# Kernel optimization log

Hardware: AMD Instinct MI355X
Metric: run time of the kernel (lower is better)

## Reference

```python
import jax, jax.numpy as jnp
import numpy as np

DIM = 1024
N_HEADS = 16
HEAD_DIM = DIM // N_HEADS
LORA_DIM = 16
B, T = 4, 1024


def _rope(x):
    # x: [B, H, T, D] with D even; rotate first/second halves (torch impl style)
    D = x.shape[-1]
    half = D // 2
    theta = 1.0 / (10000.0 ** (jnp.arange(0, D, 2, dtype=jnp.float32) / D))  # [D/2]
    pos = jnp.arange(x.shape[-2], dtype=jnp.float32)                         # [T]
    pt = pos[:, None] * theta[None, :]                                       # [T, D/2]
    sin, cos = jnp.sin(pt), jnp.cos(pt)
    xr, xi = x[..., :half], x[..., half:]
    return jnp.concatenate([xr * cos - xi * sin, xr * sin + xi * cos], axis=-1)


def setup_inputs() -> dict:
    key = jax.random.key(0)
    ks = jax.random.split(key, 16)
    def n(k, shape, std=0.02):
        return jax.random.normal(k, shape, jnp.float32) * std
    return {
        "x": jax.random.normal(ks[0], (B, T, DIM), jnp.float32),
        "q_w": n(ks[1], (DIM, DIM)),
        "k_w": n(ks[2], (DIM, DIM)),
        "v_w": n(ks[3], (DIM, DIM)),
        "q_a": n(ks[4], (LORA_DIM, DIM), 0.001),
        "q_b": n(ks[5], (DIM, LORA_DIM), 0.001),
        "q_l": jax.random.normal(ks[6], (DIM,), jnp.float32),
        "k_a": n(ks[7], (LORA_DIM, DIM), 0.001),
        "k_b": n(ks[8], (DIM, LORA_DIM), 0.001),
        "k_l": jax.random.normal(ks[9], (DIM,), jnp.float32),
        "v_a": n(ks[10], (LORA_DIM, DIM), 0.001),
        "v_b": n(ks[11], (DIM, LORA_DIM), 0.001),
        "v_l": jax.random.normal(ks[12], (DIM,), jnp.float32),
        "proj_w": n(ks[13], (DIM, DIM)),
        "proj_b": n(ks[14], (DIM,)),
    }


def reference(x, q_w, k_w, v_w, q_a, q_b, q_l, k_a, k_b, k_l,
              v_a, v_b, v_l, proj_w, proj_b):
    Bb, Tt, C = x.shape
    # token shift: xx[t] = x[t-1], xx[0] = 0 (ZeroPad2d((0,0,1,-1)))
    xx = jnp.pad(x, ((0, 0), (1, 0), (0, 0)))[:, :Tt]
    xxx = xx - x

    def lora(a, b, lam):
        return lam + jnp.tanh(x @ a.T) @ b.T  # [B,T,C]

    q = (x + xxx * lora(q_a, q_b, q_l)) @ q_w.T
    k = (x + xxx * lora(k_a, k_b, k_l)) @ k_w.T
    v = (x + xxx * lora(v_a, v_b, v_l)) @ v_w.T

    def split_heads(t):
        return t.reshape(Bb, Tt, N_HEADS, HEAD_DIM).transpose(0, 2, 1, 3)  # [B,H,T,D]

    q = _rope(split_heads(q))
    k = _rope(split_heads(k))
    v = split_heads(v)

    scale = 1.0 / np.sqrt(HEAD_DIM).astype(np.float32)
    scores = jnp.einsum('bhqd,bhkd->bhqk', q, k) * scale
    causal = jnp.tril(jnp.ones((Tt, Tt), dtype=bool))
    scores = jnp.where(causal, scores, jnp.float32(-1e30))
    att = jax.nn.softmax(scores, axis=-1)
    out = jnp.einsum('bhqk,bhkd->bhqd', att, v)
    out = out.transpose(0, 2, 1, 3).reshape(Bb, Tt, C)
    return out @ proj_w.T + proj_b
```

## Files before the change

### kernel.cpp

```cpp
#include <hip/hip_runtime.h>
#include <hip/hip_bf16.h>

typedef __hip_bfloat16 bf16;
typedef __attribute__((ext_vector_type(8))) short bf16x8;
typedef __attribute__((ext_vector_type(4))) float f32x4;

typedef const __attribute__((address_space(1))) unsigned int* gp_t;
typedef __attribute__((address_space(3))) unsigned int* lp_t;

__device__ __forceinline__ bf16 tobf(float f) { return __float2bfloat16(f); }
__device__ __forceinline__ float tof(bf16 h) { return __bfloat162float(h); }

__device__ __forceinline__ short bfbits(float f) {
    bf16 h = __float2bfloat16(f);
    return *reinterpret_cast<short*>(&h);
}
__device__ __forceinline__ bf16x8 pack8(float4 a, float4 b) {
    bf16x8 r;
    r[0] = bfbits(a.x); r[1] = bfbits(a.y); r[2] = bfbits(a.z); r[3] = bfbits(a.w);
    r[4] = bfbits(b.x); r[5] = bfbits(b.y); r[6] = bfbits(b.z); r[7] = bfbits(b.w);
    return r;
}

__device__ __forceinline__ void gload_lds16(const void* g, void* l) {
    __builtin_amdgcn_global_load_lds((gp_t)g, (lp_t)l, 16, 0, 0);
}

__global__ __launch_bounds__(256) void lora_t_wconv(
    const float* x,
    const float* qa, const float* ka, const float* va,
    const float* qw, const float* kw, const float* vw, const float* pw,
    bf16* wdst, float* Tg) {
    int tid = threadIdx.x;

    if (blockIdx.x >= 256) {
        int cblk = blockIdx.x - 256;
        int m = cblk >> 7;
        const float* src = m == 0 ? qw : (m == 1 ? kw : (m == 2 ? vw : pw));
        bf16* dst = wdst + (size_t)m * (1u << 20);
        int off = (cblk & 127) * 8192;
#pragma unroll
        for (int u = 0; u < 8; ++u) {
            int i = off + u * 1024 + tid * 4;
            float4 f = *(const float4*)(src + i);
            ushort4 o4;
            o4.x = (unsigned short)bfbits(f.x);
            o4.y = (unsigned short)bfbits(f.y);
            o4.z = (unsigned short)bfbits(f.z);
            o4.w = (unsigned short)bfbits(f.w);
            *(ushort4*)&dst[i] = o4;
        }
        return;
    }

    int wave = tid >> 6, lane = tid & 63;
    int quad = lane >> 4, l16 = lane & 15;
    int row0 = blockIdx.x * 16;
    int kb = wave * 256;

    __shared__ float spT[3][4][16][17];

    const float* xb = x + (size_t)(row0 + l16) * 1024 + kb + quad * 8;
    const float* qab = qa + (size_t)l16 * 1024 + kb + quad * 8;
    const float* kab = ka + (size_t)l16 * 1024 + kb + quad * 8;
    const float* vab = va + (size_t)l16 * 1024 + kb + quad * 8;

    f32x4 acc[3];
#pragma unroll
    for (int m = 0; m < 3; m++) acc[m] = (f32x4){0.f, 0.f, 0.f, 0.f};

#pragma unroll 2
    for (int kk = 0; kk < 256; kk += 32) {
        bf16x8 af = pack8(*(const float4*)(xb + kk), *(const float4*)(xb + kk + 4));
        bf16x8 bq = pack8(*(const float4*)(qab + kk), *(const float4*)(qab + kk + 4));
        bf16x8 bk = pack8(*(const float4*)(kab + kk), *(const float4*)(kab + kk + 4));
        bf16x8 bv = pack8(*(const float4*)(vab + kk), *(const float4*)(vab + kk + 4));
        acc[0] = __builtin_amdgcn_mfma_f32_16x16x32_bf16(af, bq, acc[0], 0, 0, 0);
        acc[1] = __builtin_amdgcn_mfma_f32_16x16x32_bf16(af, bk, acc[1], 0, 0, 0);
        acc[2] = __builtin_amdgcn_mfma_f32_16x16x32_bf16(af, bv, acc[2], 0, 0, 0);
    }

#pragma unroll
    for (int m = 0; m < 3; m++)
#pragma unroll
        for (int r = 0; r < 4; r++)
            spT[m][wave][quad * 4 + r][l16] = acc[m][r];
    __syncthreads();

    for (int i = tid; i < 768; i += 256) {
        int m = i >> 8, idx = i & 255;
        int row = idx >> 4, col = idx & 15;
        float v = spT[m][0][row][col] + spT[m][1][row][col]
                + spT[m][2][row][col] + spT[m][3][row][col];
        Tg[(size_t)(row0 + row) * 48 + m * 16 + col] = tanhf(v);
    }
}

__global__ __launch_bounds__(256) void lora_gate(
    const float* x, const float* Tg,
    const float* qbw, const float* ql,
    const float* kbw, const float* kl,
    const float* vbw, const float* vl,
    bf16* xqo, bf16* xko, bf16* xvo) {
    int tb = blockIdx.x >> 2, dc = blockIdx.x & 3;
    int row0 = tb * 32, d0 = dc * 256;
    int tid = threadIdx.x;
    int d = d0 + tid;

    __shared__ float sTT[32 * 48];

    for (int i = tid; i < 384; i += 256)
        *(float4*)&sTT[i * 4] = *(const float4*)&Tg[(size_t)row0 * 48 + i * 4];

    float qbv[16], kbv[16], vbv[16];
#pragma unroll
    for (int p = 0; p < 4; ++p) {
        *(float4*)&qbv[p * 4] = *(const float4*)(qbw + (size_t)d * 16 + p * 4);
        *(float4*)&kbv[p * 4] = *(const float4*)(kbw + (size_t)d * 16 + p * 4);
        *(float4*)&vbv[p * 4] = *(const float4*)(vbw + (size_t)d * 16 + p * 4);
    }
    float qlv = ql[d], klv = kl[d], vlv = vl[d];

    float xv[32];
#pragma unroll
    for (int i = 0; i < 32; ++i) xv[i] = x[(size_t)(row0 + i) * 1024 + d];
    int prow = (row0 == 0) ? 0 : row0 - 1;
    float xpv = x[(size_t)prow * 1024 + d];
    float xp = ((row0 & 1023) == 0) ? 0.f : xpv;

    __syncthreads();

#pragma unroll
    for (int rr = 0; rr < 32; ++rr) {
        float xc = xv[rr];
        float dx = xp - xc;
        float gq = qlv, gk = klv, gv = vlv;
#pragma unroll
        for (int p = 0; p < 4; ++p) {
            float4 tq = *(const float4*)&sTT[rr * 48 + p * 4];
            float4 tk = *(const float4*)&sTT[rr * 48 + 16 + p * 4];
            float4 tv = *(const float4*)&sTT[rr * 48 + 32 + p * 4];
            gq += tq.x * qbv[p * 4] + tq.y * qbv[p * 4 + 1] + tq.z * qbv[p * 4 + 2] + tq.w * qbv[p * 4 + 3];
            gk += tk.x * kbv[p * 4] + tk.y * kbv[p * 4 + 1] + tk.z * kbv[p * 4 + 2] + tk.w * kbv[p * 4 + 3];
            gv += tv.x * vbv[p * 4] + tv.y * vbv[p * 4 + 1] + tv.z * vbv[p * 4 + 2] + tv.w * vbv[p * 4 + 3];
        }
        size_t o = (size_t)(row0 + rr) * 1024 + d;
        xqo[o] = tobf(xc + dx * gq);
        xko[o] = tobf(xc + dx * gk);
        xvo[o] = tobf(xc + dx * gv);
        xp = xc;
    }
}

__global__ __launch_bounds__(256) void gemm128(
    const bf16* A0, const bf16* A1, const bf16* A2,
    const bf16* W0, const bf16* W1, const bf16* W2,
    bf16* C0, bf16* C1, bf16* C2,
    const float* bias, float* outF, int proj, int zcnt) {
    const int K = 1024;
    int ppx = (zcnt * 32) >> 3;
    int xcd = blockIdx.x & 7;
    int j = blockIdx.x >> 3;
    int pair = xcd * ppx + (j >> 3);
    int n0 = (j & 7) * 128;
    int bz = pair >> 5;
    int m0 = (pair & 31) * 128;

    const bf16* A = bz == 0 ? A0 : (bz == 1 ? A1 : A2);
    const bf16* W = bz == 0 ? W0 : (bz == 1 ? W1 : W2);
    bf16* C = bz == 0 ? C0 : (bz == 1 ? C1 : C2);

    __shared__ alignas(16) bf16 sA[2][64 * 64];
    __shared__ alignas(16) bf16 sB[2][64 * 64];

    int wave = threadIdx.x >> 6, lane = threadIdx.x & 63;
    int quad = lane >> 4, l16 = lane & 15;

    f32x4 acc[4][4];
#pragma unroll
    for (int i = 0; i < 4; i++)
#pragma unroll
        for (int j2 = 0; j2 < 4; j2++) acc[i][j2] = (f32x4){0.f, 0.f, 0.f, 0.f};

    int Rb0 = wave * 16 + (lane >> 3);
    int s0 = lane & 7;

    const bf16* aSrc[2];
    const bf16* bSrc[2];
#pragma unroll
    for (int p = 0; p < 2; p++) {
        int R = Rb0 + p * 8;
        int cs = s0 ^ (R & 7);
        int mr = 2 * R + (cs >> 2);
        int kc = (cs & 3) * 8;
        aSrc[p] = A + (size_t)(m0 + mr) * K + kc;
        bSrc[p] = W + (size_t)(n0 + mr) * K + kc;
    }

    auto stage = [&](int it, int bufi) {
#pragma unroll
        for (int p = 0; p < 2; p++) {
            gload_lds16(aSrc[p] + it * 32, &sA[bufi][(wave * 16 + p * 8) * 64]);
            gload_lds16(bSrc[p] + it * 32, &sB[bufi][(wave * 16 + p * 8) * 64]);
        }
    };

    int mw = (wave >> 1) * 64, nw = (wave & 1) * 64;
    int slot = (((l16 & 1) << 2) | quad) ^ ((l16 >> 1) & 7);
    int abase = ((mw >> 1) + (l16 >> 1)) * 64 + slot * 8;
    int bbase = ((nw >> 1) + (l16 >> 1)) * 64 + slot * 8;

    stage(0, 0);
    stage(1, 1);
    for (int it = 0; it < 32; ++it) {
        int buf = it & 1;
        if (it < 31) asm volatile("s_waitcnt vmcnt(4)" ::: "memory");
        else         asm volatile("s_waitcnt vmcnt(0)" ::: "memory");
        asm volatile("s_barrier" ::: "memory");
        const bf16* sAb = &sA[buf][0];
        const bf16* sBb = &sB[buf][0];
        bf16x8 af[4], bfr[4];
#pragma unroll
        for (int f = 0; f < 4; f++) {
            af[f] = *(const bf16x8*)&sAb[abase + f * 512];
            bfr[f] = *(const bf16x8*)&sBb[bbase + f * 512];
        }
#pragma unroll
        for (int i = 0; i < 4; i++)
#pragma unroll
            for (int j2 = 0; j2 < 4; j2++)
                acc[i][j2] = __builtin_amdgcn_mfma_f32_16x16x32_bf16(af[i], bfr[j2], acc[i][j2], 0, 0, 0);
        asm volatile("s_barrier" ::: "memory");
        if (it + 2 < 32) stage(it + 2, buf);
    }

    if (proj) {
#pragma unroll
        for (int i = 0; i < 4; i++) {
            int mrow = m0 + mw + i * 16 + quad * 4;
#pragma unroll
            for (int j2 = 0; j2 < 4; j2++) {
                int col = n0 + nw + j2 * 16 + l16;
                float bv = bias[col];
#pragma unroll
                for (int r = 0; r < 4; r++)
                    outF[(size_t)(mrow + r) * 1024 + col] = acc[i][j2][r] + bv;
            }
        }
    } else if (bz < 2) {
        float sc = (bz == 0) ? 0.125f : 1.0f;
        int tb = ((m0 + mw) & 1023) + quad * 4;
#pragma unroll
        for (int j2 = 0; j2 < 2; j2++) {
            int d = j2 * 16 + l16;
            float theta = __expf(-(float)d * (9.210340371976184f / 32.0f));
            float s1, c1, s16, c16, st, ct;
            sincosf(theta, &s1, &c1);
            sincosf(16.0f * theta, &s16, &c16);
            sincosf((float)tb * theta, &st, &ct);
            int col = n0 + nw + j2 * 16 + l16;
#pragma unroll
            for (int i = 0; i < 4; i++) {
                int mrow = m0 + mw + i * 16 + quad * 4;
                float c = ct, s = st;
#pragma unroll
                for (int r = 0; r < 4; r++) {
                    float xr = acc[i][j2][r], xi = acc[i][j2 + 2][r];
                    C[(size_t)(mrow + r) * 1024 + col] = tobf((xr * c - xi * s) * sc);
                    C[(size_t)(mrow + r) * 1024 + col + 32] = tobf((xr * s + xi * c) * sc);
                    float cn = c * c1 - s * s1;
                    s = s * c1 + c * s1;
                    c = cn;
                }
                float cn = ct * c16 - st * s16;
                st = st * c16 + ct * s16;
                ct = cn;
            }
        }
    } else {
#pragma unroll
        for (int i = 0; i < 4; i++) {
            int mrow = m0 + mw + i * 16 + quad * 4;
#pragma unroll
            for (int j2 = 0; j2 < 4; j2++) {
                int col = n0 + nw + j2 * 16 + l16;
                ushort4 o4;
                o4.x = (unsigned short)bfbits(acc[i][j2][0]);
                o4.y = (unsigned short)bfbits(acc[i][j2][1]);
                o4.z = (unsigned short)bfbits(acc[i][j2][2]);
                o4.w = (unsigned short)bfbits(acc[i][j2][3]);
                *(ushort4*)&C[(size_t)col * 4096 + mrow] = o4;
            }
        }
    }
}

__global__ __launch_bounds__(256) void attention(const bf16* Qm, const bf16* Km,
                                                 const bf16* Vt, bf16* attn) {
    int gid = blockIdx.x;
    int qblk = 15 - (gid >> 6);
    int bh = (((gid >> 3) & 7) << 3) | (gid & 7);
    int b = bh >> 4, h = bh & 15;
    int wave = threadIdx.x >> 6, lane = threadIdx.x & 63;
    int quad = lane >> 4, l16 = lane & 15;
    int m7 = l16 & 7;

    const bf16* Qb = Qm + (size_t)b * 1024 * 1024 + h * 64;
    const bf16* Kb = Km + (size_t)b * 1024 * 1024 + h * 64;
    const bf16* Vb = Vt + (size_t)(h * 64) * 4096 + b * 1024;

    __shared__ alignas(16) bf16 sK[2][64 * 64];
    __shared__ alignas(16) bf16 sV[2][64 * 64];
    __shared__ alignas(16) bf16 sP[4][16 * 64];

    int srow = lane >> 3;
    int scol = ((lane & 7) ^ srow) * 8;

    auto stage = [&](int kt, int bufi) {
#pragma unroll
        for (int p = 0; p < 2; p++) {
            int rbase = p * 32 + wave * 8;
            gload_lds16(Kb + (size_t)(kt * 64 + rbase + srow) * 1024 + scol, &sK[bufi][rbase * 64]);
            gload_lds16(Vb + (size_t)(rbase + srow) * 4096 + kt * 64 + scol, &sV[bufi][rbase * 64]);
        }
    };

    int qrow0 = qblk * 64 + wave * 16;
    bf16x8 aq0 = *(const bf16x8*)&Qb[(size_t)(qrow0 + l16) * 1024 + quad * 8];
    bf16x8 aq1 = *(const bf16x8*)&Qb[(size_t)(qrow0 + l16) * 1024 + quad * 8 + 32];

    f32x4 o[4];
#pragma unroll
    for (int nt = 0; nt < 4; nt++) o[nt] = (f32x4){0.f, 0.f, 0.f, 0.f};
    float lpart[4] = {0.f, 0.f, 0.f, 0.f};

    stage(0, 0);

    int buf = 0;
    for (int kt = 0; kt <= qblk; ++kt, buf ^= 1) {
        __syncthreads();
        if (kt < qblk) stage(kt + 1, buf ^ 1);

        f32x4 S[4];
#pragma unroll
        for (int j = 0; j < 4; j++) {
            int row = j * 16 + l16;
            bf16x8 bk0 = *(const bf16x8*)&sK[buf][row * 64 + ((quad ^ m7) * 8)];
            bf16x8 bk1 = *(const bf16x8*)&sK[buf][row * 64 + (((quad + 4) ^ m7) * 8)];
            f32x4 z = __builtin_amdgcn_mfma_f32_16x16x32_bf16(aq0, bk0, (f32x4){0.f, 0.f, 0.f, 0.f}, 0, 0, 0);
            S[j] = __builtin_amdgcn_mfma_f32_16x16x32_bf16(aq1, bk1, z, 0, 0, 0);
        }
        if (kt == qblk) {
#pragma unroll
            for (int j = 0; j < 4; j++) {
                int key = kt * 64 + j * 16 + l16;
#pragma unroll
                for (int r = 0; r < 4; r++) {
                    int qr = qrow0 + quad * 4 + r;
                    if (key > qr) S[j][r] = -3.0e38f;
                }
            }
        }
#pragma unroll
        for (int j = 0; j < 4; j++)
#pragma unroll
            for (int r = 0; r < 4; r++) {
                float p = __expf(S[j][r]);
                S[j][r] = p;
                lpart[r] += p;
            }

#pragma unroll
        for (int j = 0; j < 4; j++) {
            int c = j * 2 + (l16 >> 3);
#pragma unroll
            for (int r = 0; r < 4; r++) {
                int prow = quad * 4 + r;
                sP[wave][prow * 64 + ((c ^ (prow & 7)) * 8) + m7] = tobf(S[j][r]);
            }
        }
        asm volatile("s_waitcnt lgkmcnt(0)" ::: "memory");
        bf16x8 ap0 = *(const bf16x8*)&sP[wave][l16 * 64 + ((quad ^ m7) * 8)];
        bf16x8 ap1 = *(const bf16x8*)&sP[wave][l16 * 64 + (((quad + 4) ^ m7) * 8)];
#pragma unroll
        for (int nt = 0; nt < 4; nt++) {
            int row = nt * 16 + l16;
            bf16x8 bv0 = *(const bf16x8*)&sV[buf][row * 64 + ((quad ^ m7) * 8)];
            bf16x8 bv1 = *(const bf16x8*)&sV[buf][row * 64 + (((quad + 4) ^ m7) * 8)];
            o[nt] = __builtin_amdgcn_mfma_f32_16x16x32_bf16(ap0, bv0, o[nt], 0, 0, 0);
            o[nt] = __builtin_amdgcn_mfma_f32_16x16x32_bf16(ap1, bv1, o[nt], 0, 0, 0);
        }
    }

    float invl[4];
#pragma unroll
    for (int r = 0; r < 4; r++) {
        float v = lpart[r];
        v += __shfl_xor(v, 1);
        v += __shfl_xor(v, 2);
        v += __shfl_xor(v, 4);
        v += __shfl_xor(v, 8);
        invl[r] = 1.0f / v;
    }
#pragma unroll
    for (int nt = 0; nt < 4; nt++)
#pragma unroll
        for (int r = 0; r < 4; r++) {
            int t = qrow0 + quad * 4 + r;
            int col = h * 64 + nt * 16 + l16;
            attn[(size_t)(b * 1024 + t) * 1024 + col] = tobf(o[nt][r] * invl[r]);
        }
}

extern "C" void kernel_launch(void* const* d_in, const int* in_sizes, int n_in,
                              void* d_out, int out_size, void* d_ws, size_t ws_size,
                              hipStream_t stream) {
    const float* x = (const float*)d_in[0];
    const float* qw = (const float*)d_in[1];
    const float* kw = (const float*)d_in[2];
    const float* vw = (const float*)d_in[3];
    const float* qa = (const float*)d_in[4];
    const float* qb = (const float*)d_in[5];
    const float* ql = (const float*)d_in[6];
    const float* ka = (const float*)d_in[7];
    const float* kb = (const float*)d_in[8];
    const float* kl = (const float*)d_in[9];
    const float* va = (const float*)d_in[10];
    const float* vb = (const float*)d_in[11];
    const float* vl = (const float*)d_in[12];
    const float* pw = (const float*)d_in[13];
    const float* pb = (const float*)d_in[14];
    float* out = (float*)d_out;

    char* ws = (char*)d_ws;
    const size_t MB = 1024 * 1024;
    bf16* wqb = (bf16*)ws;
    bf16* wkb = wqb + 1048576;
    bf16* wvb = wkb + 1048576;
    bf16* wpb = wvb + 1048576;
    bf16* xqb = (bf16*)(ws + 8 * MB);
    bf16* xkb = xqb + 4194304;
    bf16* xvb = xkb + 4194304;
    bf16* qm = (bf16*)(ws + 32 * MB);
    bf16* km = qm + 4194304;
    bf16* Vt = km + 4194304;
    bf16* attn = xqb;
    float* Tg = (float*)(ws + 32 * MB);

    lora_t_wconv<<<768, 256, 0, stream>>>(x, qa, ka, va, qw, kw, vw, pw, wqb, Tg);
    lora_gate<<<512, 256, 0, stream>>>(x, Tg, qb, ql, kb, kl, vb, vl, xqb, xkb, xvb);
    gemm128<<<768, 256, 0, stream>>>(xqb, xkb, xvb, wqb, wkb, wvb, qm, km, Vt,
                                     nullptr, nullptr, 0, 3);
    attention<<<1024, 256, 0, stream>>>(qm, km, Vt, attn);
    gemm128<<<256, 256, 0, stream>>>(attn, nullptr, nullptr, wpb, nullptr, nullptr,
                                     nullptr, nullptr, nullptr, pb, out, 1, 1);
}
```

Measured before the change: 207.9 us.

## Load attention K/V tiles directly from global memory instead of staging through LDS

The attention kernel drops its double-buffered LDS staging of K and V tiles, along with the per-iteration __syncthreads. Each wave now reads its MFMA operands for K and V straight from global memory through precomputed per-lane pointers. This removes the barrier and LDS traffic, but the four waves in a block now each fetch the same K/V data and rely on L1/L2 to absorb the duplication, with no prefetch overlap. Separately, the GEMM kernel is templated on the projection flag so the epilogue branch is resolved at compile time.

```diff
diff --git a/kernel.cpp b/kernel.cpp
--- a/kernel.cpp
+++ b/kernel.cpp
@@ -152,11 +152,12 @@
     }
 }
 
-__global__ __launch_bounds__(256) void gemm128(
+template <int PROJ>
+__global__ __launch_bounds__(256) void gemm128t(
     const bf16* A0, const bf16* A1, const bf16* A2,
     const bf16* W0, const bf16* W1, const bf16* W2,
     bf16* C0, bf16* C1, bf16* C2,
-    const float* bias, float* outF, int proj, int zcnt) {
+    const float* bias, float* outF, int zcnt) {
     const int K = 1024;
     int ppx = (zcnt * 32) >> 3;
     int xcd = blockIdx.x & 7;
@@ -234,7 +235,7 @@
         if (it + 2 < 32) stage(it + 2, buf);
     }
 
-    if (proj) {
+    if constexpr (PROJ) {
 #pragma unroll
         for (int i = 0; i < 4; i++) {
             int mrow = m0 + mw + i * 16 + quad * 4;
@@ -309,21 +310,15 @@
     const bf16* Kb = Km + (size_t)b * 1024 * 1024 + h * 64;
     const bf16* Vb = Vt + (size_t)(h * 64) * 4096 + b * 1024;
 
-    __shared__ alignas(16) bf16 sK[2][64 * 64];
-    __shared__ alignas(16) bf16 sV[2][64 * 64];
     __shared__ alignas(16) bf16 sP[4][16 * 64];
 
-    int srow = lane >> 3;
-    int scol = ((lane & 7) ^ srow) * 8;
-
-    auto stage = [&](int kt, int bufi) {
-#pragma unroll
-        for (int p = 0; p < 2; p++) {
-            int rbase = p * 32 + wave * 8;
-            gload_lds16(Kb + (size_t)(kt * 64 + rbase + srow) * 1024 + scol, &sK[bufi][rbase * 64]);
-            gload_lds16(Vb + (size_t)(rbase + srow) * 4096 + kt * 64 + scol, &sV[bufi][rbase * 64]);
-        }
-    };
+    const bf16* kPtr[4];
+    const bf16* vPtr[4];
+#pragma unroll
+    for (int j = 0; j < 4; j++) {
+        kPtr[j] = Kb + (size_t)(j * 16 + l16) * 1024 + quad * 8;
+        vPtr[j] = Vb + (size_t)(j * 16 + l16) * 4096 + quad * 8;
+    }
 
     int qrow0 = qblk * 64 + wave * 16;
     bf16x8 aq0 = *(const bf16x8*)&Qb[(size_t)(qrow0 + l16) * 1024 + quad * 8];
@@ -334,19 +329,15 @@
     for (int nt = 0; nt < 4; nt++) o[nt] = (f32x4){0.f, 0.f, 0.f, 0.f};
     float lpart[4] = {0.f, 0.f, 0.f, 0.f};
 
-    stage(0, 0);
-
-    int buf = 0;
-    for (int kt = 0; kt <= qblk; ++kt, buf ^= 1) {
-        __syncthreads();
-        if (kt < qblk) stage(kt + 1, buf ^ 1);
+    for (int kt = 0; kt <= qblk; ++kt) {
+        size_t ko = (size_t)kt * 65536;
+        int vo = kt * 64;
 
         f32x4 S[4];
 #pragma unroll
         for (int j = 0; j < 4; j++) {
-            int row = j * 16 + l16;
-            bf16x8 bk0 = *(const bf16x8*)&sK[buf][row * 64 + ((quad ^ m7) * 8)];
-            bf16x8 bk1 = *(const bf16x8*)&sK[buf][row * 64 + (((quad + 4) ^ m7) * 8)];
+            bf16x8 bk0 = *(const bf16x8*)(kPtr[j] + ko);
+            bf16x8 bk1 = *(const bf16x8*)(kPtr[j] + ko + 32);
             f32x4 z = __builtin_amdgcn_mfma_f32_16x16x32_bf16(aq0, bk0, (f32x4){0.f, 0.f, 0.f, 0.f}, 0, 0, 0);
             S[j] = __builtin_amdgcn_mfma_f32_16x16x32_bf16(aq1, bk1, z, 0, 0, 0);
         }
@@ -384,9 +375,8 @@
         bf16x8 ap1 = *(const bf16x8*)&sP[wave][l16 * 64 + (((quad + 4) ^ m7) * 8)];
 #pragma unroll
         for (int nt = 0; nt < 4; nt++) {
-            int row = nt * 16 + l16;
-            bf16x8 bv0 = *(const bf16x8*)&sV[buf][row * 64 + ((quad ^ m7) * 8)];
-            bf16x8 bv1 = *(const bf16x8*)&sV[buf][row * 64 + (((quad + 4) ^ m7) * 8)];
+            bf16x8 bv0 = *(const bf16x8*)(vPtr[nt] + vo);
+            bf16x8 bv1 = *(const bf16x8*)(vPtr[nt] + vo + 32);
             o[nt] = __builtin_amdgcn_mfma_f32_16x16x32_bf16(ap0, bv0, o[nt], 0, 0, 0);
             o[nt] = __builtin_amdgcn_mfma_f32_16x16x32_bf16(ap1, bv1, o[nt], 0, 0, 0);
         }
@@ -449,9 +439,9 @@
 
     lora_t_wconv<<<768, 256, 0, stream>>>(x, qa, ka, va, qw, kw, vw, pw, wqb, Tg);
     lora_gate<<<512, 256, 0, stream>>>(x, Tg, qb, ql, kb, kl, vb, vl, xqb, xkb, xvb);
-    gemm128<<<768, 256, 0, stream>>>(xqb, xkb, xvb, wqb, wkb, wvb, qm, km, Vt,
-                                     nullptr, nullptr, 0, 3);
+    gemm128t<0><<<768, 256, 0, stream>>>(xqb, xkb, xvb, wqb, wkb, wvb, qm, km, Vt,
+                                         nullptr, nullptr, 3);
     attention<<<1024, 256, 0, stream>>>(qm, km, Vt, attn);
-    gemm128<<<256, 256, 0, stream>>>(attn, nullptr, nullptr, wpb, nullptr, nullptr,
-                                     nullptr, nullptr, nullptr, pb, out, 1, 1);
-}
+    gemm128t<1><<<256, 256, 0, stream>>>(attn, nullptr, nullptr, wpb, nullptr, nullptr,
+                                         nullptr, nullptr, nullptr, pb, out, 1);
+}
```

Measured after the change: 250.7 us. 20.6% more time.
